# Kernel tuning notes

Hardware: AMD Instinct MI355X
Metric: run time of the kernel (lower is better)

## Reference

```python
import jax, jax.numpy as jnp
import numpy as np

B, S, D_MODEL, K_CH, OUT = 16, 8192, 256, 256, 256


def setup_inputs() -> dict:
    key = jax.random.key(0)
    ks = jax.random.split(key, 9)
    s = lambda fan_in: 1.0 / np.sqrt(fan_in)
    return {
        "query": jax.random.normal(ks[0], (B, D_MODEL), dtype=jnp.float32),
        "key": jax.random.normal(ks[1], (B, S, K_CH), dtype=jnp.float32),
        "value": jax.random.normal(ks[2], (B, S, K_CH), dtype=jnp.float32),
        "Wq": jax.random.uniform(ks[3], (D_MODEL, OUT), jnp.float32, -s(D_MODEL), s(D_MODEL)),
        "bq": jax.random.uniform(ks[4], (OUT,), jnp.float32, -s(D_MODEL), s(D_MODEL)),
        "Wk": jax.random.uniform(ks[5], (K_CH, OUT), jnp.float32, -s(K_CH), s(K_CH)),
        "bk": jax.random.uniform(ks[6], (OUT,), jnp.float32, -s(K_CH), s(K_CH)),
        "Wv": jax.random.uniform(ks[7], (K_CH, OUT), jnp.float32, -s(K_CH), s(K_CH)),
        "bv": jax.random.uniform(ks[8], (OUT,), jnp.float32, -s(K_CH), s(K_CH)),
    }


def reference(query, key, value, Wq, bq, Wk, bk, Wv, bv):
    # q is a single vector per batch; the torch module expands it to S identical
    # rows, making every output row identical. We compute one row and broadcast
    # -- mathematically identical, O(S*d) instead of O(S^2*d).
    q = query @ Wq + bq                      # [B, OUT]
    k = jnp.einsum("bsc,co->bso", key, Wk) + bk    # [B, S, OUT]
    v = jnp.einsum("bsc,co->bso", value, Wv) + bv  # [B, S, OUT]
    scale = 1.0 / jnp.sqrt(jnp.float32(q.shape[-1]))
    scores = jnp.einsum("bo,bso->bs", q, k) * scale  # [B, S]
    w = jax.nn.softmax(scores, axis=-1)              # [B, S]
    ctx = jnp.einsum("bs,bso->bo", w, v)             # [B, OUT]
    seq_len = k.shape[1]
    return jnp.broadcast_to(ctx[:, None, :], (ctx.shape[0], seq_len, ctx.shape[1]))
```

## Files before the change

kernel.cpp:

```cpp
#include <hip/hip_runtime.h>

typedef float f4 __attribute__((ext_vector_type(4)));

constexpr int Bn = 16;
constexpr int Sn = 8192;
constexpr int Dn = 256;
constexpr float kScale = 0.0625f;
constexpr int NCHUNK = 64;
constexpr int CHUNK  = Sn / NCHUNK;

constexpr int R_OFF    = 0;
constexpr int C_OFF    = R_OFF + Bn * Dn;
constexpr int CTX_OFF  = C_OFF + 64;
constexpr int M_OFF    = CTX_OFF + Bn * Dn;
constexpr int SUM_OFF  = M_OFF + Bn * NCHUNK;
constexpr int PART_OFF = SUM_OFF + Bn * NCHUNK;

__global__ __launch_bounds__(256) void k_qrc(
    const float* __restrict__ query, const float* __restrict__ Wq,
    const float* __restrict__ bq, const float* __restrict__ Wk,
    const float* __restrict__ bk, float* __restrict__ ws) {
  int b = blockIdx.x, i = threadIdx.x;
  __shared__ float qs[Dn];
  __shared__ float qh[Dn];
  __shared__ float red[256];
  qs[i] = query[b * Dn + i];
  __syncthreads();
  float acc = bq[i];
  #pragma unroll 8
  for (int d = 0; d < Dn; ++d) acc += qs[d] * Wq[d * Dn + i];
  qh[i] = acc;
  __syncthreads();
  float racc = 0.f;
  #pragma unroll 8
  for (int o = 0; o < Dn; ++o) racc += Wk[i * Dn + o] * qh[o];
  ws[R_OFF + b * Dn + i] = racc;
  red[i] = qh[i] * bk[i];
  __syncthreads();
  for (int off = 128; off; off >>= 1) {
    if (i < off) red[i] += red[i + off];
    __syncthreads();
  }
  if (i == 0) ws[C_OFF + b] = red[0];
}

__global__ __launch_bounds__(256) void k_fused(
    const float* __restrict__ key, const float* __restrict__ value,
    float* __restrict__ ws) {
  int blk = blockIdx.x;
  int b = blk >> 6;
  int chunk = blk & 63;
  int s0 = chunk * CHUNK;
  int t = threadIdx.x, lane = t & 63, wv = t >> 6;
  __shared__ float sc[CHUNK];
  __shared__ float wsh[CHUNK];
  __shared__ float red[4][Dn];

  f4 rv = ((const f4*)(ws + R_OFF + b * Dn))[lane];
  float cb = ws[C_OFF + b];
  const f4* kp = (const f4*)(key + ((size_t)b * Sn + s0) * Dn);
  const f4* vp = (const f4*)(value + ((size_t)b * Sn + s0) * Dn);

  #pragma unroll 4
  for (int i = 0; i < CHUNK / 4; ++i) {
    int sl = wv + 4 * i;
    f4 kv = __builtin_nontemporal_load(&kp[(size_t)sl * 64 + lane]);
    float dot = kv.x * rv.x + kv.y * rv.y + kv.z * rv.z + kv.w * rv.w;
    #pragma unroll
    for (int off = 32; off; off >>= 1) dot += __shfl_xor(dot, off, 64);
    if (lane == 0) sc[sl] = (dot + cb) * kScale;
  }
  __syncthreads();

  float m = -1e30f;
  #pragma unroll 8
  for (int i = 0; i < CHUNK; ++i) m = fmaxf(m, sc[i]);
  if (t < CHUNK) wsh[t] = __expf(sc[t] - m);
  __syncthreads();

  f4 acc = {0.f, 0.f, 0.f, 0.f};
  #pragma unroll 4
  for (int i = 0; i < CHUNK / 4; ++i) {
    int sl = wv + 4 * i;
    f4 v = __builtin_nontemporal_load(&vp[(size_t)sl * 64 + lane]);
    float w = wsh[sl];
    acc.x += w * v.x; acc.y += w * v.y; acc.z += w * v.z; acc.w += w * v.w;
  }
  red[wv][lane * 4 + 0] = acc.x;
  red[wv][lane * 4 + 1] = acc.y;
  red[wv][lane * 4 + 2] = acc.z;
  red[wv][lane * 4 + 3] = acc.w;
  __syncthreads();
  float part = red[0][t] + red[1][t] + red[2][t] + red[3][t];
  ws[PART_OFF + ((size_t)b * NCHUNK + chunk) * Dn + t] = part;
  if (t == 0) {
    float ssum = 0.f;
    #pragma unroll 8
    for (int i = 0; i < CHUNK; ++i) ssum += wsh[i];
    ws[M_OFF + b * NCHUNK + chunk] = m;
    ws[SUM_OFF + b * NCHUNK + chunk] = ssum;
  }
}

__global__ __launch_bounds__(256) void k_combine(
    const float* __restrict__ Wv, const float* __restrict__ bv,
    float* __restrict__ ws) {
  int b = blockIdx.x, t = threadIdx.x;
  __shared__ float msh[NCHUNK];
  __shared__ float e[NCHUNK];
  __shared__ float ush[Dn];
  if (t < NCHUNK) msh[t] = ws[M_OFF + b * NCHUNK + t];
  __syncthreads();
  float gm = -1e30f;
  #pragma unroll 8
  for (int c = 0; c < NCHUNK; ++c) gm = fmaxf(gm, msh[c]);
  if (t < NCHUNK) e[t] = __expf(msh[t] - gm);
  __syncthreads();
  float denom = 0.f;
  #pragma unroll 8
  for (int c = 0; c < NCHUNK; ++c) denom += ws[SUM_OFF + b * NCHUNK + c] * e[c];
  float u = 0.f;
  #pragma unroll 8
  for (int c = 0; c < NCHUNK; ++c)
    u += ws[PART_OFF + ((size_t)b * NCHUNK + c) * Dn + t] * e[c];
  ush[t] = u / denom;
  __syncthreads();
  float acc = bv[t];
  #pragma unroll 8
  for (int o = 0; o < Dn; ++o) acc += ush[o] * Wv[o * Dn + t];
  ws[CTX_OFF + b * Dn + t] = acc;
}

__global__ __launch_bounds__(256) void k_bcast(
    const float* __restrict__ ws, float* __restrict__ out) {
  int b = blockIdx.x >> 7;
  int sb = blockIdx.x & 127;
  int t = threadIdx.x, lane = t & 63, wv = t >> 6;
  f4 val = ((const f4*)(ws + CTX_OFF + b * Dn))[lane];
  f4* op = (f4*)(out + ((size_t)b * Sn + sb * 64) * Dn);
  #pragma unroll
  for (int it = 0; it < 16; ++it) {
    int sl = wv + 4 * it;
    __builtin_nontemporal_store(val, &op[(size_t)sl * 64 + lane]);
  }
}

extern "C" void kernel_launch(void* const* d_in, const int* in_sizes, int n_in,
                              void* d_out, int out_size, void* d_ws, size_t ws_size,
                              hipStream_t stream) {
  const float* query = (const float*)d_in[0];
  const float* key   = (const float*)d_in[1];
  const float* value = (const float*)d_in[2];
  const float* Wq    = (const float*)d_in[3];
  const float* bq    = (const float*)d_in[4];
  const float* Wk    = (const float*)d_in[5];
  const float* bk    = (const float*)d_in[6];
  const float* Wv    = (const float*)d_in[7];
  const float* bv    = (const float*)d_in[8];
  float* out = (float*)d_out;
  float* ws  = (float*)d_ws;

  hipLaunchKernelGGL(k_qrc,     dim3(Bn),          dim3(256), 0, stream,
                     query, Wq, bq, Wk, bk, ws);
  hipLaunchKernelGGL(k_fused,   dim3(Bn * NCHUNK), dim3(256), 0, stream,
                     key, value, ws);
  hipLaunchKernelGGL(k_combine, dim3(Bn),          dim3(256), 0, stream,
                     Wv, bv, ws);
  hipLaunchKernelGGL(k_bcast,   dim3(Bn * 128),    dim3(256), 0, stream, ws, out);
}
```

Baseline: 106.8 us.

## Fuse query projection into chunk kernel and combine into broadcast kernel

```diff
diff --git a/kernel.cpp b/kernel.cpp
--- a/kernel.cpp
+++ b/kernel.cpp
@@ -9,42 +9,14 @@
 constexpr int NCHUNK = 64;
 constexpr int CHUNK  = Sn / NCHUNK;
 
-constexpr int R_OFF    = 0;
-constexpr int C_OFF    = R_OFF + Bn * Dn;
-constexpr int CTX_OFF  = C_OFF + 64;
-constexpr int M_OFF    = CTX_OFF + Bn * Dn;
+constexpr int M_OFF    = 0;
 constexpr int SUM_OFF  = M_OFF + Bn * NCHUNK;
 constexpr int PART_OFF = SUM_OFF + Bn * NCHUNK;
 
-__global__ __launch_bounds__(256) void k_qrc(
+__global__ __launch_bounds__(256) void k_fused(
     const float* __restrict__ query, const float* __restrict__ Wq,
     const float* __restrict__ bq, const float* __restrict__ Wk,
-    const float* __restrict__ bk, float* __restrict__ ws) {
-  int b = blockIdx.x, i = threadIdx.x;
-  __shared__ float qs[Dn];
-  __shared__ float qh[Dn];
-  __shared__ float red[256];
-  qs[i] = query[b * Dn + i];
-  __syncthreads();
-  float acc = bq[i];
-  #pragma unroll 8
-  for (int d = 0; d < Dn; ++d) acc += qs[d] * Wq[d * Dn + i];
-  qh[i] = acc;
-  __syncthreads();
-  float racc = 0.f;
-  #pragma unroll 8
-  for (int o = 0; o < Dn; ++o) racc += Wk[i * Dn + o] * qh[o];
-  ws[R_OFF + b * Dn + i] = racc;
-  red[i] = qh[i] * bk[i];
-  __syncthreads();
-  for (int off = 128; off; off >>= 1) {
-    if (i < off) red[i] += red[i + off];
-    __syncthreads();
-  }
-  if (i == 0) ws[C_OFF + b] = red[0];
-}
-
-__global__ __launch_bounds__(256) void k_fused(
+    const float* __restrict__ bk,
     const float* __restrict__ key, const float* __restrict__ value,
     float* __restrict__ ws) {
   int blk = blockIdx.x;
@@ -52,12 +24,36 @@
   int chunk = blk & 63;
   int s0 = chunk * CHUNK;
   int t = threadIdx.x, lane = t & 63, wv = t >> 6;
+
+  __shared__ float qs[Dn];
+  __shared__ float qh[Dn];
+  __shared__ float rsh[Dn];
   __shared__ float sc[CHUNK];
   __shared__ float wsh[CHUNK];
   __shared__ float red[4][Dn];
+  float* redf = &red[0][0];
 
-  f4 rv = ((const f4*)(ws + R_OFF + b * Dn))[lane];
-  float cb = ws[C_OFF + b];
+  qs[t] = query[b * Dn + t];
+  __syncthreads();
+  float acc = bq[t];
+  #pragma unroll 8
+  for (int d = 0; d < Dn; ++d) acc += qs[d] * Wq[d * Dn + t];
+  qh[t] = acc;
+  __syncthreads();
+  float racc = 0.f;
+  #pragma unroll 8
+  for (int o = 0; o < Dn; ++o) racc += Wk[t * Dn + o] * qh[o];
+  rsh[t] = racc;
+  redf[t] = qh[t] * bk[t];
+  __syncthreads();
+  for (int off = 128; off; off >>= 1) {
+    if (t < off) redf[t] += redf[t + off];
+    __syncthreads();
+  }
+  float cb = redf[0];
+  __syncthreads();
+  f4 rv = ((const f4*)rsh)[lane];
+
   const f4* kp = (const f4*)(key + ((size_t)b * Sn + s0) * Dn);
   const f4* vp = (const f4*)(value + ((size_t)b * Sn + s0) * Dn);
 
@@ -78,18 +74,18 @@
   if (t < CHUNK) wsh[t] = __expf(sc[t] - m);
   __syncthreads();
 
-  f4 acc = {0.f, 0.f, 0.f, 0.f};
+  f4 vacc = {0.f, 0.f, 0.f, 0.f};
   #pragma unroll 4
   for (int i = 0; i < CHUNK / 4; ++i) {
     int sl = wv + 4 * i;
     f4 v = __builtin_nontemporal_load(&vp[(size_t)sl * 64 + lane]);
     float w = wsh[sl];
-    acc.x += w * v.x; acc.y += w * v.y; acc.z += w * v.z; acc.w += w * v.w;
+    vacc.x += w * v.x; vacc.y += w * v.y; vacc.z += w * v.z; vacc.w += w * v.w;
   }
-  red[wv][lane * 4 + 0] = acc.x;
-  red[wv][lane * 4 + 1] = acc.y;
-  red[wv][lane * 4 + 2] = acc.z;
-  red[wv][lane * 4 + 3] = acc.w;
+  red[wv][lane * 4 + 0] = vacc.x;
+  red[wv][lane * 4 + 1] = vacc.y;
+  red[wv][lane * 4 + 2] = vacc.z;
+  red[wv][lane * 4 + 3] = vacc.w;
   __syncthreads();
   float part = red[0][t] + red[1][t] + red[2][t] + red[3][t];
   ws[PART_OFF + ((size_t)b * NCHUNK + chunk) * Dn + t] = part;
@@ -102,13 +98,20 @@
   }
 }
 
-__global__ __launch_bounds__(256) void k_combine(
+__global__ __launch_bounds__(256) void k_out(
     const float* __restrict__ Wv, const float* __restrict__ bv,
-    float* __restrict__ ws) {
-  int b = blockIdx.x, t = threadIdx.x;
+    const float* __restrict__ ws, float* __restrict__ out) {
+  int blk = blockIdx.x;
+  int b = blk >> 6;
+  int chunk = blk & 63;
+  int s0 = chunk * CHUNK;
+  int t = threadIdx.x, lane = t & 63, wv = t >> 6;
+
   __shared__ float msh[NCHUNK];
   __shared__ float e[NCHUNK];
   __shared__ float ush[Dn];
+  __shared__ float ctx[Dn];
+
   if (t < NCHUNK) msh[t] = ws[M_OFF + b * NCHUNK + t];
   __syncthreads();
   float gm = -1e30f;
@@ -128,18 +131,13 @@
   float acc = bv[t];
   #pragma unroll 8
   for (int o = 0; o < Dn; ++o) acc += ush[o] * Wv[o * Dn + t];
-  ws[CTX_OFF + b * Dn + t] = acc;
-}
+  ctx[t] = acc;
+  __syncthreads();
 
-__global__ __launch_bounds__(256) void k_bcast(
-    const float* __restrict__ ws, float* __restrict__ out) {
-  int b = blockIdx.x >> 7;
-  int sb = blockIdx.x & 127;
-  int t = threadIdx.x, lane = t & 63, wv = t >> 6;
-  f4 val = ((const f4*)(ws + CTX_OFF + b * Dn))[lane];
-  f4* op = (f4*)(out + ((size_t)b * Sn + sb * 64) * Dn);
-  #pragma unroll
-  for (int it = 0; it < 16; ++it) {
+  f4 val = ((const f4*)ctx)[lane];
+  f4* op = (f4*)(out + ((size_t)b * Sn + s0) * Dn);
+  #pragma unroll 8
+  for (int it = 0; it < CHUNK / 4; ++it) {
     int sl = wv + 4 * it;
     __builtin_nontemporal_store(val, &op[(size_t)sl * 64 + lane]);
   }
@@ -160,11 +158,8 @@
   float* out = (float*)d_out;
   float* ws  = (float*)d_ws;
 
-  hipLaunchKernelGGL(k_qrc,     dim3(Bn),          dim3(256), 0, stream,
-                     query, Wq, bq, Wk, bk, ws);
-  hipLaunchKernelGGL(k_fused,   dim3(Bn * NCHUNK), dim3(256), 0, stream,
-                     key, value, ws);
-  hipLaunchKernelGGL(k_combine, dim3(Bn),          dim3(256), 0, stream,
-                     Wv, bv, ws);
-  hipLaunchKernelGGL(k_bcast,   dim3(Bn * 128),    dim3(256), 0, stream, ws, out);
+  hipLaunchKernelGGL(k_fused, dim3(Bn * NCHUNK), dim3(256), 0, stream,
+                     query, Wq, bq, Wk, bk, key, value, ws);
+  hipLaunchKernelGGL(k_out,   dim3(Bn * NCHUNK), dim3(256), 0, stream,
+                     Wv, bv, ws, out);
 }
```

Result: slower. 141.2 us (+32.3%).
